# Optimization experiments

Measured on AMD Instinct MI355X. Metric: run time of the kernel, lower is better.

The kernel has to match this reference:

```python
import jax, jax.numpy as jnp
import numpy as np

B, H, W, C = 32, 112, 112, 96
NH, WS, SHIFT = 3, 7, 3
HID = 4 * C
N = WS * WS
HD = C // NH


def setup_inputs() -> dict:
    key = jax.random.key(0)
    ks = jax.random.split(key, 8)
    s = 0.02
    inp = {}
    inp['x'] = jax.random.normal(ks[0], (B, H * W, C), jnp.float32)
    # --- standard Swin shift attention mask ---
    img = np.zeros((1, H, W, 1), np.float32)
    cnt = 0
    for hs in (slice(0, -WS), slice(-WS, -SHIFT), slice(-SHIFT, None)):
        for wsl in (slice(0, -WS), slice(-WS, -SHIFT), slice(-SHIFT, None)):
            img[:, hs, wsl, :] = cnt
            cnt += 1
    mw = img.reshape(1, H // WS, WS, W // WS, WS, 1).transpose(0, 1, 3, 2, 4, 5).reshape(-1, N)
    am = mw[:, None, :] - mw[:, :, None]
    inp['attn_mask'] = jnp.asarray(np.where(am != 0, -100.0, 0.0).astype(np.float32))
    # --- relative position index ---
    coords = np.stack(np.meshgrid(np.arange(WS), np.arange(WS), indexing='ij'))  # (2, ws, ws)
    cf = coords.reshape(2, -1)
    rel = (cf[:, :, None] - cf[:, None, :]).transpose(1, 2, 0)  # (N, N, 2)
    rel[:, :, 0] += WS - 1
    rel[:, :, 1] += WS - 1
    rel[:, :, 0] *= 2 * WS - 1
    inp['rel_index'] = jnp.asarray(rel.sum(-1).astype(np.int32))  # (N, N)
    # --- params ---
    inp['norm1_g'] = jnp.ones((C,), jnp.float32)
    inp['norm1_b'] = jnp.zeros((C,), jnp.float32)
    inp['qkv_w'] = jax.random.normal(ks[1], (3 * C, C), jnp.float32) * s
    inp['qkv_b'] = jnp.zeros((3 * C,), jnp.float32)
    inp['proj_w'] = jax.random.normal(ks[2], (C, C), jnp.float32) * s
    inp['proj_b'] = jnp.zeros((C,), jnp.float32)
    inp['rel_bias_table'] = jax.random.normal(ks[3], ((2 * WS - 1) ** 2, NH), jnp.float32) * s
    inp['norm2_g'] = jnp.ones((C,), jnp.float32)
    inp['norm2_b'] = jnp.zeros((C,), jnp.float32)
    inp['fc1_w'] = jax.random.normal(ks[4], (HID, C), jnp.float32) * s
    inp['fc1_b'] = jnp.zeros((HID,), jnp.float32)
    inp['fc2_w'] = jax.random.normal(ks[5], (C, HID), jnp.float32) * s
    inp['fc2_b'] = jnp.zeros((C,), jnp.float32)
    return inp


def _ln(x, g, b):
    m = x.mean(-1, keepdims=True)
    v = ((x - m) ** 2).mean(-1, keepdims=True)
    return (x - m) * jax.lax.rsqrt(v + 1e-5) * g + b


def reference(x, attn_mask, rel_index, norm1_g, norm1_b, qkv_w, qkv_b, proj_w, proj_b,
              rel_bias_table, norm2_g, norm2_b, fc1_w, fc1_b, fc2_w, fc2_b):
    b = x.shape[0]
    shortcut = x
    h = _ln(x, norm1_g, norm1_b).reshape(b, H, W, C)
    # H, W divisible by WS -> pad is a no-op; cyclic shift
    h = jnp.roll(h, (-SHIFT, -SHIFT), axis=(1, 2))
    nWh, nWw = H // WS, W // WS
    nW = nWh * nWw
    # window partition -> (b*nW, N, C)
    xw = h.reshape(b, nWh, WS, nWw, WS, C).transpose(0, 1, 3, 2, 4, 5).reshape(-1, N, C)
    qkv = (xw @ qkv_w.T + qkv_b).reshape(-1, N, 3, NH, HD).transpose(2, 0, 3, 1, 4)
    q, k, v = qkv[0], qkv[1], qkv[2]  # each (b*nW, NH, N, HD)
    q = q * (HD ** -0.5)
    attn = jnp.einsum('whnd,whmd->whnm', q, k)  # (b*nW, NH, N, N)
    bias = rel_bias_table[rel_index.reshape(-1)].reshape(N, N, NH).transpose(2, 0, 1)
    attn = attn + bias[None]
    attn = attn.reshape(b, nW, NH, N, N) + attn_mask[None, :, None]
    attn = jax.nn.softmax(attn, axis=-1).reshape(-1, NH, N, N)
    out = jnp.einsum('whnm,whmd->whnd', attn, v).transpose(0, 2, 1, 3).reshape(-1, N, C)
    out = out @ proj_w.T + proj_b
    # window reverse + reverse shift
    out = out.reshape(b, nWh, nWw, WS, WS, C).transpose(0, 1, 3, 2, 4, 5).reshape(b, H, W, C)
    out = jnp.roll(out, (SHIFT, SHIFT), axis=(1, 2)).reshape(b, H * W, C)
    x1 = shortcut + out
    y = _ln(x1, norm2_g, norm2_b)
    y = jax.nn.gelu(y @ fc1_w.T + fc1_b, approximate=False) @ fc2_w.T + fc2_b
    return x1 + y
```

## Files before the change

### kernel.cpp

```cpp
#include <hip/hip_runtime.h>
#include <hip/hip_bf16.h>
#include <math.h>

#define HH 112
#define WW_ 112
#define CC 96
#define NHH 3
#define WSZ 7
#define SHIFT_ 3
#define NTOK 49
#define HDIM 32
#define WTOT 8192
#define MTOT 401408
#define QKS 204
#define H1S 76
#define VTS 68

#define WQ_SZ (288 * 104)
#define WP_SZ (96 * 104)
#define W1_SZ (384 * 104)
#define W2_SZ (6 * 96 * 72)
#define WPAD_TOT (WQ_SZ + WP_SZ + W1_SZ + W2_SZ)
#define BOF_QKV 0
#define BOF_PROJ 288
#define BOF_FC1 384
#define BOF_FC2 768
#define BOF_G1 864
#define BOF_B1 960
#define BOF_G2 1056
#define BOF_B2 1152
#define BIAS_TOT 1248

typedef __hip_bfloat16 bf16;
typedef __attribute__((ext_vector_type(8))) short short8;
typedef __attribute__((ext_vector_type(4))) float floatx4;

static __device__ __forceinline__ short f2bits(float v) {
  bf16 h = __float2bfloat16(v);
  short s;
  __builtin_memcpy(&s, &h, 2);
  return s;
}
static __device__ __forceinline__ float bf2f(bf16 v) { return __bfloat162float(v); }
static __device__ __forceinline__ bf16 f2bf(float v) { return __float2bfloat16(v); }

template <typename T> struct IO;
template <> struct IO<float> {
  static __device__ __forceinline__ float ld(const float* p, long i) { return p[i]; }
  static __device__ __forceinline__ void st(float* p, long i, float v) { p[i] = v; }
};
template <> struct IO<bf16> {
  static __device__ __forceinline__ float ld(const bf16* p, long i) { return bf2f(p[i]); }
  static __device__ __forceinline__ void st(bf16* p, long i, float v) { p[i] = f2bf(v); }
};

__global__ void detect_kernel(const unsigned short* __restrict__ x, int* flag) {
  __shared__ int tot;
  if (threadIdx.x == 0) tot = 0;
  __syncthreads();
  int bad = 0;
  for (int i = threadIdx.x; i < 8192; i += 256) {
    int e = (x[i] >> 7) & 0xFF;
    if (e >= 0x86) bad++;
  }
  atomicAdd(&tot, bad);
  __syncthreads();
  if (threadIdx.x == 0) *flag = (tot > 64) ? 1 : 0;
}

template <typename T>
__device__ __forceinline__ void prep_body(
    const T* qkv_w, const T* proj_w, const T* fc1_w, const T* fc2_w,
    const T* qkv_b, const T* proj_b, const T* fc1_b, const T* fc2_b,
    const T* g1, const T* b1, const T* g2, const T* b2,
    bf16* wpad, float* bias) {
  int idx = blockIdx.x * 256 + threadIdx.x;
  if (idx < WQ_SZ) {
    int r = idx / 104, c = idx % 104;
    wpad[idx] = (c < CC) ? f2bf(IO<T>::ld(qkv_w, (long)r * CC + c)) : f2bf(0.f);
  } else if (idx < WQ_SZ + WP_SZ) {
    int j = idx - WQ_SZ;
    int r = j / 104, c = j % 104;
    wpad[idx] = (c < CC) ? f2bf(IO<T>::ld(proj_w, (long)r * CC + c)) : f2bf(0.f);
  } else if (idx < WQ_SZ + WP_SZ + W1_SZ) {
    int j = idx - (WQ_SZ + WP_SZ);
    int r = j / 104, c = j % 104;
    wpad[idx] = (c < CC) ? f2bf(IO<T>::ld(fc1_w, (long)r * CC + c)) : f2bf(0.f);
  } else if (idx < WPAD_TOT) {
    int j = idx - (WQ_SZ + WP_SZ + W1_SZ);
    int ch = j / (96 * 72), rem = j % (96 * 72);
    int r = rem / 72, c = rem % 72;
    wpad[idx] = (c < 64) ? f2bf(IO<T>::ld(fc2_w, (long)r * (4 * CC) + ch * 64 + c))
                         : f2bf(0.f);
  } else if (idx < WPAD_TOT + BIAS_TOT) {
    int j = idx - WPAD_TOT;
    float v;
    if (j < 288) v = IO<T>::ld(qkv_b, j);
    else if (j < 384) v = IO<T>::ld(proj_b, j - 288);
    else if (j < 768) v = IO<T>::ld(fc1_b, j - 384);
    else if (j < 864) v = IO<T>::ld(fc2_b, j - 768);
    else if (j < 960) v = IO<T>::ld(g1, j - 864);
    else if (j < 1056) v = IO<T>::ld(b1, j - 960);
    else if (j < 1152) v = IO<T>::ld(g2, j - 1056);
    else v = IO<T>::ld(b2, j - 1152);
    bias[j] = v;
  }
}
__global__ __launch_bounds__(256) void prep_kernel(
    const int* __restrict__ flag, const void* qkv_w, const void* proj_w,
    const void* fc1_w, const void* fc2_w, const void* qkv_b, const void* proj_b,
    const void* fc1_b, const void* fc2_b, const void* g1, const void* b1,
    const void* g2, const void* b2, bf16* __restrict__ wpad,
    float* __restrict__ bias) {
  if (*flag)
    prep_body<float>((const float*)qkv_w, (const float*)proj_w, (const float*)fc1_w,
                     (const float*)fc2_w, (const float*)qkv_b, (const float*)proj_b,
                     (const float*)fc1_b, (const float*)fc2_b, (const float*)g1,
                     (const float*)b1, (const float*)g2, (const float*)b2, wpad, bias);
  else
    prep_body<bf16>((const bf16*)qkv_w, (const bf16*)proj_w, (const bf16*)fc1_w,
                    (const bf16*)fc2_w, (const bf16*)qkv_b, (const bf16*)proj_b,
                    (const bf16*)fc1_b, (const bf16*)fc2_b, (const bf16*)g1,
                    (const bf16*)b1, (const bf16*)g2, (const bf16*)b2, wpad, bias);
}

template <typename T>
__device__ __forceinline__ void combine_body(const T* mask, const int* rel,
                                             const T* bt, bf16* comb) {
  long idx = (long)blockIdx.x * 256 + threadIdx.x;
  long rem = idx % 7203;
  long wi = idx / 7203;
  int h = (int)(rem / 2401);
  int n2 = (int)(rem % 2401);
  float v = IO<T>::ld(bt, (long)rel[n2] * NHH + h) + IO<T>::ld(mask, wi * 2401 + n2);
  comb[idx] = f2bf(v);
}
__global__ __launch_bounds__(256) void combine_kernel(
    const int* __restrict__ flag, const void* mask, const int* __restrict__ rel,
    const void* bt, bf16* __restrict__ comb) {
  if (*flag)
    combine_body<float>((const float*)mask, rel, (const float*)bt, comb);
  else
    combine_body<bf16>((const bf16*)mask, rel, (const bf16*)bt, comb);
}

template <typename T>
__device__ __forceinline__ void qkv_attn_body(
    const T* x, const bf16* wq, const float* bias, const bf16* comb,
    bf16* attn_out, short* qk, short* R, short* wc) {
  int win = blockIdx.x;
  int wave = threadIdx.x >> 6;
  int lane = threadIdx.x & 63;
  int col = lane & 15, kg = lane >> 4;
  {
    int r = lane >> 2;
    int seg = lane & 3;
    int n = wave * 16 + r;
    short* dst = R + n * 104 + seg * 24;
    if (n < NTOK) {
      int bq_ = win >> 8, wi = win & 255;
      int wh = wi >> 4, ww = wi & 15;
      int i = n / WSZ, j = n - (n / WSZ) * WSZ;
      int hs = wh * WSZ + i + SHIFT_; if (hs >= HH) hs -= HH;
      int ws = ww * WSZ + j + SHIFT_; if (ws >= WW_) ws -= WW_;
      const T* src = x + ((long)bq_ * (HH * WW_) + (long)hs * WW_ + ws) * CC + seg * 24;
      float a[24];
#pragma unroll
      for (int t = 0; t < 24; ++t) a[t] = IO<T>::ld(src, t);
      float s = 0.f;
#pragma unroll
      for (int t = 0; t < 24; ++t) s += a[t];
      s += __shfl_xor(s, 1, 64);
      s += __shfl_xor(s, 2, 64);
      float mean = s * (1.f / CC);
      float var = 0.f;
#pragma unroll
      for (int t = 0; t < 24; ++t) { float d = a[t] - mean; var += d * d; }
      var += __shfl_xor(var, 1, 64);
      var += __shfl_xor(var, 2, 64);
      float rstd = rsqrtf(var * (1.f / CC) + 1e-5f);
      const float* gg = bias + BOF_G1 + seg * 24;
      const float* bb = bias + BOF_B1 + seg * 24;
#pragma unroll
      for (int t = 0; t < 24; ++t)
        dst[t] = f2bits((a[t] - mean) * rstd * gg[t] + bb[t]);
    } else {
#pragma unroll
      for (int t = 0; t < 24; ++t) dst[t] = 0;
    }
  }
  short8 af[3];
#pragma unroll
  for (int kc = 0; kc < 3; ++kc)
    af[kc] = *(const short8*)(R + (wave * 16 + col) * 104 + kc * 32 + kg * 8);
  const float scale = 0.17677669529663687f;
  for (int c = 0; c < 6; ++c) {
    __syncthreads();
    {
      const float4* src = (const float4*)(wq + c * 48 * 104);
      float4* dst = (float4*)wc;
      for (int i = threadIdx.x; i < 624; i += 256) dst[i] = src[i];
    }
    __syncthreads();
#pragma unroll
    for (int t = 0; t < 3; ++t) {
      floatx4 acc = {0.f, 0.f, 0.f, 0.f};
#pragma unroll
      for (int kc = 0; kc < 3; ++kc) {
        short8 bfr = *(const short8*)(wc + (t * 16 + col) * 104 + kc * 32 + kg * 8);
        acc = __builtin_amdgcn_mfma_f32_16x16x32_bf16(af[kc], bfr, acc, 0, 0, 0);
      }
      int nc = c * 3 + t;
      int cc = nc * 16 + col;
      float bb = bias[BOF_QKV + cc];
      if (nc < 6) {
#pragma unroll
        for (int r = 0; r < 4; ++r)
          qk[(wave * 16 + kg * 4 + r) * QKS + cc] = f2bits((acc[r] + bb) * scale);
      } else if (nc < 12) {
#pragma unroll
        for (int r = 0; r < 4; ++r)
          qk[(wave * 16 + kg * 4 + r) * QKS + cc] = f2bits(acc[r] + bb);
      } else {
        int d = cc - 2 * CC;
#pragma unroll
        for (int r = 0; r < 4; ++r)
          R[d * VTS + wave * 16 + kg * 4 + r] = f2bits(acc[r] + bb);
      }
    }
  }
  __syncthreads();
  floatx4 st[3][4];
#pragma unroll
  for (int h = 0; h < NHH; ++h) {
    short8 qa = *(const short8*)(qk + (wave * 16 + col) * QKS + h * HDIM + kg * 8);
#pragma unroll
    for (int nt = 0; nt < 4; ++nt) {
      short8 kb = *(const short8*)(qk + (nt * 16 + col) * QKS + CC + h * HDIM + kg * 8);
      floatx4 z = {0.f, 0.f, 0.f, 0.f};
      st[h][nt] = __builtin_amdgcn_mfma_f32_16x16x32_bf16(qa, kb, z, 0, 0, 0);
    }
  }
  __syncthreads();
  const bf16* cb = comb + (long)(win & 255) * (NHH * 2401);
#pragma unroll
  for (int h = 0; h < NHH; ++h) {
#pragma unroll
    for (int r = 0; r < 4; ++r) {
      int m = wave * 16 + kg * 4 + r;
      int mc = (m < NTOK) ? m : (NTOK - 1);
      float sv[4];
      float mx = -1e30f;
#pragma unroll
      for (int nt = 0; nt < 4; ++nt) {
        int n = nt * 16 + col;
        float v = (n < NTOK)
                      ? (st[h][nt][r] + bf2f(cb[h * 2401 + mc * NTOK + n]))
                      : -1e30f;
        sv[nt] = v;
        mx = fmaxf(mx, v);
      }
#pragma unroll
      for (int msk = 1; msk < 16; msk <<= 1) mx = fmaxf(mx, __shfl_xor(mx, msk, 64));
      float sum = 0.f;
#pragma unroll
      for (int nt = 0; nt < 4; ++nt) {
        float e = __expf(sv[nt] - mx);
        sv[nt] = e;
        sum += e;
      }
#pragma unroll
      for (int msk = 1; msk < 16; msk <<= 1) sum += __shfl_xor(sum, msk, 64);
      float inv = 1.f / sum;
#pragma unroll
      for (int nt = 0; nt < 4; ++nt)
        qk[m * QKS + h * 64 + nt * 16 + col] = f2bits(sv[nt] * inv);
    }
  }
#pragma unroll
  for (int h = 0; h < NHH; ++h) {
    floatx4 oa[2];
    oa[0] = (floatx4){0.f, 0.f, 0.f, 0.f};
    oa[1] = (floatx4){0.f, 0.f, 0.f, 0.f};
#pragma unroll
    for (int kc = 0; kc < 2; ++kc) {
      short8 pa = *(const short8*)(qk + (wave * 16 + col) * QKS + h * 64 + kc * 32 + kg * 8);
#pragma unroll
      for (int dt = 0; dt < 2; ++dt) {
        short8 vb = *(const short8*)(R + (h * HDIM + dt * 16 + col) * VTS + kc * 32 + kg * 8);
        oa[dt] = __builtin_amdgcn_mfma_f32_16x16x32_bf16(pa, vb, oa[dt], 0, 0, 0);
      }
    }
#pragma unroll
    for (int dt = 0; dt < 2; ++dt)
#pragma unroll
      for (int r = 0; r < 4; ++r) {
        int m = wave * 16 + kg * 4 + r;
        if (m < NTOK)
          attn_out[((long)win * NTOK + m) * CC + h * HDIM + dt * 16 + col] =
              f2bf(oa[dt][r]);
      }
  }
}
__global__ __launch_bounds__(256) void qkv_attn_kernel(
    const int* __restrict__ flag, const void* x, const bf16* __restrict__ wq,
    const float* __restrict__ bias, const bf16* __restrict__ comb,
    bf16* __restrict__ attn_out) {
  __shared__ short qk[64 * QKS];
  __shared__ short R[6656];
  __shared__ short wc[48 * 104];
  if (*flag)
    qkv_attn_body<float>((const float*)x, wq, bias, comb, attn_out, qk, R, wc);
  else
    qkv_attn_body<bf16>((const bf16*)x, wq, bias, comb, attn_out, qk, R, wc);
}

static __device__ __forceinline__ long scatter_index(long m) {
  int win = (int)(m / NTOK);
  int n = (int)(m - (long)win * NTOK);
  int bq = win >> 8, wi = win & 255;
  int wh = wi >> 4, ww = wi & 15;
  int i = n / WSZ, j = n - (n / WSZ) * WSZ;
  int hf = wh * WSZ + i + SHIFT_; if (hf >= HH) hf -= HH;
  int wf = ww * WSZ + j + SHIFT_; if (wf >= WW_) wf -= WW_;
  return ((long)bq * (HH * WW_) + (long)hf * WW_ + wf) * CC;
}

template <typename T>
__device__ __forceinline__ void proj_body(const bf16* A, const bf16* wp,
                                          const float* bias, T* out,
                                          const T* res, short* wl) {
  {
    const float4* src = (const float4*)wp;
    float4* dst = (float4*)wl;
    for (int i = threadIdx.x; i < 1248; i += 256) dst[i] = src[i];
  }
  __syncthreads();
  int wave = threadIdx.x >> 6;
  int lane = threadIdx.x & 63;
  int col = lane & 15;
  int kg = lane >> 4;
  long mbase = (long)blockIdx.x * 128 + wave * 32;
  short8 a0[3], a1[3];
#pragma unroll
  for (int kc = 0; kc < 3; ++kc) {
    a0[kc] = *(const short8*)(A + (mbase + col) * CC + kc * 32 + kg * 8);
    a1[kc] = *(const short8*)(A + (mbase + 16 + col) * CC + kc * 32 + kg * 8);
  }
  long dst0[4], dst1[4];
#pragma unroll
  for (int r = 0; r < 4; ++r) {
    dst0[r] = scatter_index(mbase + kg * 4 + r);
    dst1[r] = scatter_index(mbase + 16 + kg * 4 + r);
  }
#pragma unroll
  for (int nc = 0; nc < 6; ++nc) {
    floatx4 acc0 = {0.f, 0.f, 0.f, 0.f};
    floatx4 acc1 = {0.f, 0.f, 0.f, 0.f};
#pragma unroll
    for (int kc = 0; kc < 3; ++kc) {
      short8 bfr = *(const short8*)(wl + (nc * 16 + col) * 104 + kc * 32 + kg * 8);
      acc0 = __builtin_amdgcn_mfma_f32_16x16x32_bf16(a0[kc], bfr, acc0, 0, 0, 0);
      acc1 = __builtin_amdgcn_mfma_f32_16x16x32_bf16(a1[kc], bfr, acc1, 0, 0, 0);
    }
    int cc = nc * 16 + col;
    float bb = bias[BOF_PROJ + cc];
#pragma unroll
    for (int r = 0; r < 4; ++r) {
      long p0 = dst0[r] + cc;
      long p1 = dst1[r] + cc;
      IO<T>::st(out, p0, acc0[r] + bb + IO<T>::ld(res, p0));
      IO<T>::st(out, p1, acc1[r] + bb + IO<T>::ld(res, p1));
    }
  }
}
__global__ __launch_bounds__(256) void proj_kernel(
    const int* __restrict__ flag, const bf16* __restrict__ A,
    const bf16* __restrict__ wp, const float* __restrict__ bias, void* out,
    const void* res) {
  __shared__ short wl[96 * 104];
  if (*flag)
    proj_body<float>(A, wp, bias, (float*)out, (const float*)res, wl);
  else
    proj_body<bf16>(A, wp, bias, (bf16*)out, (const bf16*)res, wl);
}

template <typename T>
__device__ __forceinline__ void mlp_body(const bf16* w1, const bf16* w2,
                                         const float* bias, T* xo, short* xln,
                                         short* w1c, short* w2c) {
  int wave = threadIdx.x >> 6;
  int lane = threadIdx.x & 63;
  int col = lane & 15;
  int kg = lane >> 4;
  long mbase = (long)blockIdx.x * 64;
  {
    int r = lane >> 2;
    int seg = lane & 3;
    const T* src = xo + (mbase + wave * 16 + r) * CC + seg * 24;
    float a[24];
#pragma unroll
    for (int t = 0; t < 24; ++t) a[t] = IO<T>::ld(src, t);
    float s = 0.f;
#pragma unroll
    for (int t = 0; t < 24; ++t) s += a[t];
    s += __shfl_xor(s, 1, 64);
    s += __shfl_xor(s, 2, 64);
    float mean = s * (1.f / CC);
    float var = 0.f;
#pragma unroll
    for (int t = 0; t < 24; ++t) { float d = a[t] - mean; var += d * d; }
    var += __shfl_xor(var, 1, 64);
    var += __shfl_xor(var, 2, 64);
    float rstd = rsqrtf(var * (1.f / CC) + 1e-5f);
    const float* gg = bias + BOF_G2 + seg * 24;
    const float* bb = bias + BOF_B2 + seg * 24;
    short* dst = xln + (wave * 16 + r) * 104 + seg * 24;
#pragma unroll
    for (int t = 0; t < 24; ++t)
      dst[t] = f2bits((a[t] - mean) * rstd * gg[t] + bb[t]);
  }
  short8 af[3];
#pragma unroll
  for (int kc = 0; kc < 3; ++kc)
    af[kc] = *(const short8*)(xln + (wave * 16 + col) * 104 + kc * 32 + kg * 8);
  short* h1c = xln;
  floatx4 acc2[6];
#pragma unroll
  for (int i = 0; i < 6; ++i) acc2[i] = (floatx4){0.f, 0.f, 0.f, 0.f};
  for (int c = 0; c < 6; ++c) {
    __syncthreads();
    {
      const float4* s1 = (const float4*)(w1 + c * 64 * 104);
      float4* d1 = (float4*)w1c;
      for (int i = threadIdx.x; i < 832; i += 256) d1[i] = s1[i];
      const float4* s2 = (const float4*)(w2 + c * 96 * 72);
      float4* d2 = (float4*)w2c;
      for (int i = threadIdx.x; i < 864; i += 256) d2[i] = s2[i];
    }
    __syncthreads();
#pragma unroll
    for (int t = 0; t < 4; ++t) {
      floatx4 acc = {0.f, 0.f, 0.f, 0.f};
#pragma unroll
      for (int kc = 0; kc < 3; ++kc) {
        short8 bfr = *(const short8*)(w1c + (t * 16 + col) * 104 + kc * 32 + kg * 8);
        acc = __builtin_amdgcn_mfma_f32_16x16x32_bf16(af[kc], bfr, acc, 0, 0, 0);
      }
      float bb = bias[BOF_FC1 + c * 64 + t * 16 + col];
#pragma unroll
      for (int r = 0; r < 4; ++r) {
        float v = acc[r] + bb;
        float ge = 0.5f * v * (1.f + erff(v * 0.70710678118654752f));
        h1c[(wave * 16 + kg * 4 + r) * H1S + t * 16 + col] = f2bits(ge);
      }
    }
    short8 a2[2];
#pragma unroll
    for (int kk = 0; kk < 2; ++kk)
      a2[kk] = *(const short8*)(h1c + (wave * 16 + col) * H1S + kk * 32 + kg * 8);
#pragma unroll
    for (int nc2 = 0; nc2 < 6; ++nc2) {
#pragma unroll
      for (int kk = 0; kk < 2; ++kk) {
        short8 b2f = *(const short8*)(w2c + (nc2 * 16 + col) * 72 + kk * 32 + kg * 8);
        acc2[nc2] = __builtin_amdgcn_mfma_f32_16x16x32_bf16(a2[kk], b2f, acc2[nc2], 0, 0, 0);
      }
    }
  }
#pragma unroll
  for (int nc2 = 0; nc2 < 6; ++nc2) {
    int cc = nc2 * 16 + col;
    float bb = bias[BOF_FC2 + cc];
#pragma unroll
    for (int r = 0; r < 4; ++r) {
      long p = (mbase + wave * 16 + kg * 4 + r) * CC + cc;
      IO<T>::st(xo, p, acc2[nc2][r] + bb + IO<T>::ld(xo, p));
    }
  }
}
__global__ __launch_bounds__(256, 4) void mlp_kernel(
    const int* __restrict__ flag, const bf16* __restrict__ w1,
    const bf16* __restrict__ w2, const float* __restrict__ bias, void* xo) {
  __shared__ short xln[64 * 104];
  __shared__ short w1c[64 * 104];
  __shared__ short w2c[96 * 72];
  if (*flag)
    mlp_body<float>(w1, w2, bias, (float*)xo, xln, w1c, w2c);
  else
    mlp_body<bf16>(w1, w2, bias, (bf16*)xo, xln, w1c, w2c);
}

extern "C" void kernel_launch(void* const* d_in, const int* in_sizes, int n_in,
                              void* d_out, int out_size, void* d_ws, size_t ws_size,
                              hipStream_t stream) {
  (void)in_sizes; (void)n_in; (void)out_size; (void)ws_size;
  char* ws = (char*)d_ws;
  bf16* bufA = (bf16*)ws;
  size_t offComb = (size_t)MTOT * CC * 2;
  bf16* comb = (bf16*)(ws + offComb);
  size_t offW = offComb + (size_t)256 * NHH * 2401 * 2;
  bf16* wpad = (bf16*)(ws + offW);
  size_t offB = offW + (size_t)WPAD_TOT * 2;
  float* bias = (float*)(ws + offB);
  int* flag = (int*)(ws + offB + (size_t)BIAS_TOT * 4);

  detect_kernel<<<1, 256, 0, stream>>>((const unsigned short*)d_in[0], flag);
  prep_kernel<<<(WPAD_TOT + BIAS_TOT + 255) / 256, 256, 0, stream>>>(
      flag, d_in[5], d_in[7], d_in[12], d_in[14], d_in[6], d_in[8], d_in[13],
      d_in[15], d_in[3], d_in[4], d_in[10], d_in[11], wpad, bias);
  combine_kernel<<<7203, 256, 0, stream>>>(flag, d_in[1], (const int*)d_in[2],
                                           d_in[9], comb);
  qkv_attn_kernel<<<WTOT, 256, 0, stream>>>(flag, d_in[0], wpad, bias, comb, bufA);
  proj_kernel<<<MTOT / 128, 256, 0, stream>>>(flag, bufA, wpad + WQ_SZ, bias,
                                              d_out, d_in[0]);
  mlp_kernel<<<MTOT / 64, 256, 0, stream>>>(flag, wpad + WQ_SZ + WP_SZ,
                                            wpad + WQ_SZ + WP_SZ + W1_SZ, bias,
                                            d_out);
}
```

Measured before the change: 893.5 us.

## Read weight fragments directly from global memory instead of staging in LDS

Removes the shared-memory staging of the QKV, proj, fc1 and fc2 weights. MFMA B-fragments are now read straight from global memory, where the small weight matrices should stay L1/L2-resident. This drops the per-chunk copy loops and the barriers around them, cuts LDS use, and raises the launch-bounds occupancy hints (mlp to 8 blocks per CU). The trade-off is more global load traffic and latency per MFMA, with no explicit reuse through LDS, and the higher occupancy hints may force register limits.

```diff
diff --git a/kernel.cpp b/kernel.cpp
--- a/kernel.cpp
+++ b/kernel.cpp
@@ -147,7 +147,7 @@
 template <typename T>
 __device__ __forceinline__ void qkv_attn_body(
     const T* x, const bf16* wq, const float* bias, const bf16* comb,
-    bf16* attn_out, short* qk, short* R, short* wc) {
+    bf16* attn_out, short* qk, short* R) {
   int win = blockIdx.x;
   int wave = threadIdx.x >> 6;
   int lane = threadIdx.x & 63;
@@ -194,40 +194,36 @@
   for (int kc = 0; kc < 3; ++kc)
     af[kc] = *(const short8*)(R + (wave * 16 + col) * 104 + kc * 32 + kg * 8);
   const float scale = 0.17677669529663687f;
-  for (int c = 0; c < 6; ++c) {
-    __syncthreads();
-    {
-      const float4* src = (const float4*)(wq + c * 48 * 104);
-      float4* dst = (float4*)wc;
-      for (int i = threadIdx.x; i < 624; i += 256) dst[i] = src[i];
-    }
-    __syncthreads();
-#pragma unroll
-    for (int t = 0; t < 3; ++t) {
-      floatx4 acc = {0.f, 0.f, 0.f, 0.f};
-#pragma unroll
-      for (int kc = 0; kc < 3; ++kc) {
-        short8 bfr = *(const short8*)(wc + (t * 16 + col) * 104 + kc * 32 + kg * 8);
-        acc = __builtin_amdgcn_mfma_f32_16x16x32_bf16(af[kc], bfr, acc, 0, 0, 0);
-      }
-      int nc = c * 3 + t;
-      int cc = nc * 16 + col;
-      float bb = bias[BOF_QKV + cc];
-      if (nc < 6) {
-#pragma unroll
-        for (int r = 0; r < 4; ++r)
-          qk[(wave * 16 + kg * 4 + r) * QKS + cc] = f2bits((acc[r] + bb) * scale);
-      } else if (nc < 12) {
-#pragma unroll
-        for (int r = 0; r < 4; ++r)
-          qk[(wave * 16 + kg * 4 + r) * QKS + cc] = f2bits(acc[r] + bb);
-      } else {
-        int d = cc - 2 * CC;
-#pragma unroll
-        for (int r = 0; r < 4; ++r)
-          R[d * VTS + wave * 16 + kg * 4 + r] = f2bits(acc[r] + bb);
-      }
-    }
+#pragma unroll
+  for (int nc = 0; nc < 12; ++nc) {
+    floatx4 acc = {0.f, 0.f, 0.f, 0.f};
+#pragma unroll
+    for (int kc = 0; kc < 3; ++kc) {
+      short8 bfr = *(const short8*)(wq + (nc * 16 + col) * 104 + kc * 32 + kg * 8);
+      acc = __builtin_amdgcn_mfma_f32_16x16x32_bf16(af[kc], bfr, acc, 0, 0, 0);
+    }
+    int cc = nc * 16 + col;
+    float bb = bias[BOF_QKV + cc];
+    float m = (nc < 6) ? scale : 1.f;
+#pragma unroll
+    for (int r = 0; r < 4; ++r)
+      qk[(wave * 16 + kg * 4 + r) * QKS + cc] = f2bits((acc[r] + bb) * m);
+  }
+  __syncthreads();
+#pragma unroll
+  for (int nc = 12; nc < 18; ++nc) {
+    floatx4 acc = {0.f, 0.f, 0.f, 0.f};
+#pragma unroll
+    for (int kc = 0; kc < 3; ++kc) {
+      short8 bfr = *(const short8*)(wq + (nc * 16 + col) * 104 + kc * 32 + kg * 8);
+      acc = __builtin_amdgcn_mfma_f32_16x16x32_bf16(af[kc], bfr, acc, 0, 0, 0);
+    }
+    int cc = nc * 16 + col;
+    float bb = bias[BOF_QKV + cc];
+    int d = cc - 2 * CC;
+#pragma unroll
+    for (int r = 0; r < 4; ++r)
+      R[d * VTS + wave * 16 + kg * 4 + r] = f2bits(acc[r] + bb);
   }
   __syncthreads();
   floatx4 st[3][4];
@@ -302,17 +298,16 @@
       }
   }
 }
-__global__ __launch_bounds__(256) void qkv_attn_kernel(
+__global__ __launch_bounds__(256, 4) void qkv_attn_kernel(
     const int* __restrict__ flag, const void* x, const bf16* __restrict__ wq,
     const float* __restrict__ bias, const bf16* __restrict__ comb,
     bf16* __restrict__ attn_out) {
   __shared__ short qk[64 * QKS];
   __shared__ short R[6656];
-  __shared__ short wc[48 * 104];
   if (*flag)
-    qkv_attn_body<float>((const float*)x, wq, bias, comb, attn_out, qk, R, wc);
+    qkv_attn_body<float>((const float*)x, wq, bias, comb, attn_out, qk, R);
   else
-    qkv_attn_body<bf16>((const bf16*)x, wq, bias, comb, attn_out, qk, R, wc);
+    qkv_attn_body<bf16>((const bf16*)x, wq, bias, comb, attn_out, qk, R);
 }
 
 static __device__ __forceinline__ long scatter_index(long m) {
@@ -329,13 +324,7 @@
 template <typename T>
 __device__ __forceinline__ void proj_body(const bf16* A, const bf16* wp,
                                           const float* bias, T* out,
-                                          const T* res, short* wl) {
-  {
-    const float4* src = (const float4*)wp;
-    float4* dst = (float4*)wl;
-    for (int i = threadIdx.x; i < 1248; i += 256) dst[i] = src[i];
-  }
-  __syncthreads();
+                                          const T* res) {
   int wave = threadIdx.x >> 6;
   int lane = threadIdx.x & 63;
   int col = lane & 15;
@@ -359,7 +348,7 @@
     floatx4 acc1 = {0.f, 0.f, 0.f, 0.f};
 #pragma unroll
     for (int kc = 0; kc < 3; ++kc) {
-      short8 bfr = *(const short8*)(wl + (nc * 16 + col) * 104 + kc * 32 + kg * 8);
+      short8 bfr = *(const short8*)(wp + (nc * 16 + col) * 104 + kc * 32 + kg * 8);
       acc0 = __builtin_amdgcn_mfma_f32_16x16x32_bf16(a0[kc], bfr, acc0, 0, 0, 0);
       acc1 = __builtin_amdgcn_mfma_f32_16x16x32_bf16(a1[kc], bfr, acc1, 0, 0, 0);
     }
@@ -374,21 +363,19 @@
     }
   }
 }
-__global__ __launch_bounds__(256) void proj_kernel(
+__global__ __launch_bounds__(256, 4) void proj_kernel(
     const int* __restrict__ flag, const bf16* __restrict__ A,
     const bf16* __restrict__ wp, const float* __restrict__ bias, void* out,
     const void* res) {
-  __shared__ short wl[96 * 104];
   if (*flag)
-    proj_body<float>(A, wp, bias, (float*)out, (const float*)res, wl);
+    proj_body<float>(A, wp, bias, (float*)out, (const float*)res);
   else
-    proj_body<bf16>(A, wp, bias, (bf16*)out, (const bf16*)res, wl);
+    proj_body<bf16>(A, wp, bias, (bf16*)out, (const bf16*)res);
 }
 
 template <typename T>
 __device__ __forceinline__ void mlp_body(const bf16* w1, const bf16* w2,
-                                         const float* bias, T* xo, short* xln,
-                                         short* w1c, short* w2c) {
+                                         const float* bias, T* xo, short* xln) {
   int wave = threadIdx.x >> 6;
   int lane = threadIdx.x & 63;
   int col = lane & 15;
@@ -424,27 +411,19 @@
 #pragma unroll
   for (int kc = 0; kc < 3; ++kc)
     af[kc] = *(const short8*)(xln + (wave * 16 + col) * 104 + kc * 32 + kg * 8);
+  __syncthreads();
   short* h1c = xln;
   floatx4 acc2[6];
 #pragma unroll
   for (int i = 0; i < 6; ++i) acc2[i] = (floatx4){0.f, 0.f, 0.f, 0.f};
   for (int c = 0; c < 6; ++c) {
-    __syncthreads();
-    {
-      const float4* s1 = (const float4*)(w1 + c * 64 * 104);
-      float4* d1 = (float4*)w1c;
-      for (int i = threadIdx.x; i < 832; i += 256) d1[i] = s1[i];
-      const float4* s2 = (const float4*)(w2 + c * 96 * 72);
-      float4* d2 = (float4*)w2c;
-      for (int i = threadIdx.x; i < 864; i += 256) d2[i] = s2[i];
-    }
-    __syncthreads();
 #pragma unroll
     for (int t = 0; t < 4; ++t) {
       floatx4 acc = {0.f, 0.f, 0.f, 0.f};
 #pragma unroll
       for (int kc = 0; kc < 3; ++kc) {
-        short8 bfr = *(const short8*)(w1c + (t * 16 + col) * 104 + kc * 32 + kg * 8);
+        short8 bfr =
+            *(const short8*)(w1 + (c * 64 + t * 16 + col) * 104 + kc * 32 + kg * 8);
         acc = __builtin_amdgcn_mfma_f32_16x16x32_bf16(af[kc], bfr, acc, 0, 0, 0);
       }
       float bb = bias[BOF_FC1 + c * 64 + t * 16 + col];
@@ -463,7 +442,8 @@
     for (int nc2 = 0; nc2 < 6; ++nc2) {
 #pragma unroll
       for (int kk = 0; kk < 2; ++kk) {
-        short8 b2f = *(const short8*)(w2c + (nc2 * 16 + col) * 72 + kk * 32 + kg * 8);
+        short8 b2f = *(const short8*)(w2 + c * (96 * 72) + (nc2 * 16 + col) * 72 +
+                                      kk * 32 + kg * 8);
         acc2[nc2] = __builtin_amdgcn_mfma_f32_16x16x32_bf16(a2[kk], b2f, acc2[nc2], 0, 0, 0);
       }
     }
@@ -479,16 +459,14 @@
     }
   }
 }
-__global__ __launch_bounds__(256, 4) void mlp_kernel(
+__global__ __launch_bounds__(256, 8) void mlp_kernel(
     const int* __restrict__ flag, const bf16* __restrict__ w1,
     const bf16* __restrict__ w2, const float* __restrict__ bias, void* xo) {
   __shared__ short xln[64 * 104];
-  __shared__ short w1c[64 * 104];
-  __shared__ short w2c[96 * 72];
   if (*flag)
-    mlp_body<float>(w1, w2, bias, (float*)xo, xln, w1c, w2c);
+    mlp_body<float>(w1, w2, bias, (float*)xo, xln);
   else
-    mlp_body<bf16>(w1, w2, bias, (bf16*)xo, xln, w1c, w2c);
+    mlp_body<bf16>(w1, w2, bias, (bf16*)xo, xln);
 }
 
 extern "C" void kernel_launch(void* const* d_in, const int* in_sizes, int n_in,
```

Measured after the change: 1.042 ms. +16.7%, slower.
